# Optimization experiments

Measured on AMD Instinct MI355X. Metric: run time of the kernel, lower is better.

The kernel has to match this reference:

```python
import jax, jax.numpy as jnp
import numpy as np

NUM_ROUTING = 3
EPS = 1e-8


def squash(s, axis):
    # s * (||s||^2 / (1 + ||s||^2)) / ||s||  along `axis`
    sq = jnp.sum(s * s, axis=axis, keepdims=True)
    return s * (sq / (1.0 + sq)) / jnp.sqrt(sq + EPS)


def setup_inputs() -> dict:
    key = jax.random.key(0)
    k1, k2 = jax.random.split(key)
    B, R, C, OUT, IN = 32, 2048, 32, 32, 16
    x = jax.random.normal(k1, (B, R, IN), dtype=jnp.float32)
    vote = jax.random.normal(k2, (R, C, OUT, IN), dtype=jnp.float32)
    return {"x": x, "vote": vote}


def reference(x, vote):
    # votes[b,r,c,o] = sum_i vote[r,c,o,i] * x[b,r,i]
    votes = jnp.einsum('rcoi,bri->brco', vote, x)  # [B,R,C,OUT]
    agreement = jnp.zeros_like(votes)
    verdict = None
    for _ in range(NUM_ROUTING):
        chairman = jax.nn.softmax(agreement, axis=1)          # softmax over routes
        summary = jnp.sum(chairman * votes, axis=1, keepdims=True)  # [B,1,C,OUT]
        verdict = squash(summary, axis=3)                     # squash over out_dim
        agreement = agreement + jnp.sum(votes * verdict, axis=3, keepdims=True)
    return verdict[:, 0, :, :]  # [B, C, OUT]
```

## Files before the change

### kernel.cpp

```cpp
#include <hip/hip_runtime.h>
#include <hip/hip_fp16.h>

#define B 32
#define R 2048
#define C 32
#define O 32
#define IN 16


__global__ __launch_bounds__(512) void votes_kernel(
    const float* __restrict__ x,
    const float* __restrict__ vote,
    __half* __restrict__ votes_h)
{
  const int r0 = blockIdx.x * 16;
  const int c = blockIdx.y;
  const int t = threadIdx.x;
  const int o = t & 31;
  const int rl = t >> 5;
  const int r = r0 + rl;

  __shared__ unsigned int x_lds[32 * 16 * 12];

#pragma unroll
  for (int k = 0; k < 4; ++k) {
    int j = t + k * 512;
    int bb = j >> 6;
    int rr = (j >> 2) & 15;
    int ic = j & 3;
    float4 v = *reinterpret_cast<const float4*>(
        x + ((size_t)bb * R + r0 + rr) * IN + ic * 4);
    __half2 h01 = __float22half2_rn(make_float2(v.x, v.y));
    __half2 h23 = __float22half2_rn(make_float2(v.z, v.w));
    int w = (bb * 16 + rr) * 12 + 2 * ic;
    x_lds[w] = __builtin_bit_cast(unsigned int, h01);
    x_lds[w + 1] = __builtin_bit_cast(unsigned int, h23);
  }
  __syncthreads();

  const float4* vp = reinterpret_cast<const float4*>(
      vote + (((size_t)r * C + c) * O + o) * IN);
  float4 f0 = vp[0], f1 = vp[1], f2 = vp[2], f3 = vp[3];

  __half* optr = votes_h + (size_t)c * 65536 +
                 (size_t)(r >> 1) * 64 + o * 2 + (r & 1);

#pragma unroll 2
  for (int bb = 0; bb < 32; ++bb) {
    const unsigned int* xr = &x_lds[(bb * 16 + rl) * 12];
    uint4 xa = *reinterpret_cast<const uint4*>(xr);
    uint4 xb = *reinterpret_cast<const uint4*>(xr + 4);
    __half2 h0 = __builtin_bit_cast(__half2, xa.x);
    __half2 h1 = __builtin_bit_cast(__half2, xa.y);
    __half2 h2 = __builtin_bit_cast(__half2, xa.z);
    __half2 h3 = __builtin_bit_cast(__half2, xa.w);
    __half2 h4 = __builtin_bit_cast(__half2, xb.x);
    __half2 h5 = __builtin_bit_cast(__half2, xb.y);
    __half2 h6 = __builtin_bit_cast(__half2, xb.z);
    __half2 h7 = __builtin_bit_cast(__half2, xb.w);
    float acc =
        f0.x * __low2float(h0) + f0.y * __high2float(h0) +
        f0.z * __low2float(h1) + f0.w * __high2float(h1) +
        f1.x * __low2float(h2) + f1.y * __high2float(h2) +
        f1.z * __low2float(h3) + f1.w * __high2float(h3) +
        f2.x * __low2float(h4) + f2.y * __high2float(h4) +
        f2.z * __low2float(h5) + f2.w * __high2float(h5) +
        f3.x * __low2float(h6) + f3.y * __high2float(h6) +
        f3.z * __low2float(h7) + f3.w * __high2float(h7);
    optr[(size_t)bb * C * 65536] = __float2half(acc);
  }
}

__global__ __launch_bounds__(1024, 4) void routing_kernel(
    const __half* __restrict__ votes_h,
    float* __restrict__ out)
{
  const int b = blockIdx.x >> 5;
  const int c = blockIdx.x & 31;
  const int t = threadIdx.x;
  const int lane = t & 63;
  const int wave = t >> 6;
  const int g = t >> 5;
  const int o = t & 31;

  __shared__ unsigned int vmix[1024 * 34];
  __shared__ float2 e2[1024];
  __shared__ float red[32][33];
  __shared__ float vdf[32];
  __shared__ float scal_m[16], scal_z[16];

  const uint4* src = reinterpret_cast<const uint4*>(
      votes_h + ((size_t)b * C + c) * 65536);
#pragma unroll
  for (int k = 0; k < 8; ++k) {
    int j = t + k * 1024;
    uint4 v = src[j];
    int rp = j >> 3;
    int q = j & 7;
    unsigned int* dst = &vmix[rp * 34 + 4 * q];
    uint2 a; a.x = v.x; a.y = v.y;
    uint2 d; d.x = v.z; d.y = v.w;
    *reinterpret_cast<uint2*>(dst) = a;
    *reinterpret_cast<uint2*>(dst + 2) = d;
  }
  __syncthreads();

  float a0 = 0.0f, a1 = 0.0f;

  for (int iter = 0; iter < 3; ++iter) {
    float m = fmaxf(a0, a1);
#pragma unroll
    for (int mask = 32; mask; mask >>= 1) m = fmaxf(m, __shfl_xor(m, mask));
    if (lane == 0) scal_m[wave] = m;
    __syncthreads();
    float M = scal_m[0];
#pragma unroll
    for (int w = 1; w < 16; ++w) M = fmaxf(M, scal_m[w]);

    float e0 = __expf(a0 - M), e1 = __expf(a1 - M);
    {
      float z = e0 + e1;
#pragma unroll
      for (int mask = 32; mask; mask >>= 1) z += __shfl_xor(z, mask);
      if (lane == 0) scal_z[wave] = z;
    }
    e2[t] = make_float2(e0, e1);
    __syncthreads();
    float Z = 0.0f;
#pragma unroll
    for (int w = 0; w < 16; ++w) Z += scal_z[w];
    const float Zinv = 1.0f / Z;

    {
      float s = 0.0f;
      const unsigned int* vb = &vmix[(size_t)g * 32 * 34 + o];
      const float2* eb = &e2[g * 32];
#pragma unroll
      for (int j = 0; j < 32; ++j) {
        __half2 vv = __builtin_bit_cast(__half2, vb[j * 34]);
        float2 ee = eb[j];
        s += ee.x * __low2float(vv) + ee.y * __high2float(vv);
      }
      red[o][g] = s;
    }
    __syncthreads();

    if (t < 32) {
      float S = 0.0f;
#pragma unroll
      for (int gg = 0; gg < 32; ++gg) S += red[t][gg];
      float summary = S * Zinv;
      float sq = summary * summary;
#pragma unroll
      for (int mask = 16; mask; mask >>= 1) sq += __shfl_xor(sq, mask);
      float scale = sq / ((1.0f + sq) * sqrtf(sq + 1e-8f));
      float vd = summary * scale;
      vdf[t] = vd;
      if (iter == 2) out[((size_t)b * C + c) * O + t] = vd;
    }
    __syncthreads();

    if (iter < 2) {
      float u0 = 0.0f, u1 = 0.0f;
      const unsigned int* vb = &vmix[(size_t)t * 34];
#pragma unroll
      for (int q = 0; q < 16; ++q) {
        uint2 vv = *reinterpret_cast<const uint2*>(vb + 2 * q);
        __half2 va = __builtin_bit_cast(__half2, vv.x);
        __half2 vbh = __builtin_bit_cast(__half2, vv.y);
        float vda = vdf[2 * q], vdb = vdf[2 * q + 1];
        u0 += __low2float(va) * vda + __low2float(vbh) * vdb;
        u1 += __high2float(va) * vda + __high2float(vbh) * vdb;
      }
      a0 += u0;
      a1 += u1;
      __syncthreads();
    }
  }
}

extern "C" void kernel_launch(void* const* d_in, const int* in_sizes, int n_in,
                              void* d_out, int out_size, void* d_ws, size_t ws_size,
                              hipStream_t stream) {
  const float* x = (const float*)d_in[0];
  const float* vote = (const float*)d_in[1];
  float* out = (float*)d_out;
  __half* votes_h = (__half*)d_ws;

  votes_kernel<<<dim3(R / 16, C), 512, 0, stream>>>(x, vote, votes_h);
  routing_kernel<<<dim3(B * C), 1024, 0, stream>>>(votes_h, out);
}
```

Baseline: 284.3 us.

## Register-tile votes kernel with fp16 dot2 and drop softmax max reduction

The votes kernel now has each thread compute a 2-route by 2-output tile. Vote weights are converted to half once and kept in registers, and the inner product uses the packed fp16 dot2 instruction. Results are written as packed 8-byte stores, and each block covers 2 capsules and 32 routes. In routing, the first iteration uses a uniform softmax with no exp or reduction. The max-subtraction pass and one barrier per iteration are removed, on the assumption that agreement logits stay small enough for an unshifted exp. That removes numerical safety for large logits, and the fp16 weight conversion adds rounding error.

```diff
diff --git a/kernel.cpp b/kernel.cpp
--- a/kernel.cpp
+++ b/kernel.cpp
@@ -7,67 +7,85 @@
 #define O 32
 #define IN 16
 
-
-__global__ __launch_bounds__(512) void votes_kernel(
+typedef _Float16 hf2 __attribute__((ext_vector_type(2)));
+
+
+__global__ __launch_bounds__(512, 4) void votes_kernel(
     const float* __restrict__ x,
     const float* __restrict__ vote,
     __half* __restrict__ votes_h)
 {
-  const int r0 = blockIdx.x * 16;
-  const int c = blockIdx.y;
   const int t = threadIdx.x;
-  const int o = t & 31;
-  const int rl = t >> 5;
-  const int r = r0 + rl;
-
-  __shared__ unsigned int x_lds[32 * 16 * 12];
-
-#pragma unroll
-  for (int k = 0; k < 4; ++k) {
+  const int c = blockIdx.y * 2 + (t >> 8);
+  const int tt = t & 255;
+  const int rp_l = tt >> 4;
+  const int op = tt & 15;
+  const int r0 = blockIdx.x * 32;
+  const int r = r0 + 2 * rp_l;
+  const int rpg = blockIdx.x * 16 + rp_l;
+
+  __shared__ unsigned int x_lds[32 * 32 * 8];
+
+#pragma unroll
+  for (int k = 0; k < 8; ++k) {
     int j = t + k * 512;
-    int bb = j >> 6;
-    int rr = (j >> 2) & 15;
+    int bb = j >> 7;
+    int rr = (j >> 2) & 31;
     int ic = j & 3;
     float4 v = *reinterpret_cast<const float4*>(
         x + ((size_t)bb * R + r0 + rr) * IN + ic * 4);
     __half2 h01 = __float22half2_rn(make_float2(v.x, v.y));
     __half2 h23 = __float22half2_rn(make_float2(v.z, v.w));
-    int w = (bb * 16 + rr) * 12 + 2 * ic;
+    int w = (bb * 32 + rr) * 8 + 2 * ic;
     x_lds[w] = __builtin_bit_cast(unsigned int, h01);
     x_lds[w + 1] = __builtin_bit_cast(unsigned int, h23);
   }
+
+  unsigned int wh[4][8];
+#pragma unroll
+  for (int p = 0; p < 2; ++p) {
+#pragma unroll
+    for (int q = 0; q < 2; ++q) {
+      const float4* vp = reinterpret_cast<const float4*>(
+          vote + (((size_t)(r + p) * C + c) * O + 2 * op + q) * IN);
+#pragma unroll
+      for (int k = 0; k < 4; ++k) {
+        float4 f = vp[k];
+        __half2 a = __float22half2_rn(make_float2(f.x, f.y));
+        __half2 d = __float22half2_rn(make_float2(f.z, f.w));
+        wh[p * 2 + q][2 * k] = __builtin_bit_cast(unsigned int, a);
+        wh[p * 2 + q][2 * k + 1] = __builtin_bit_cast(unsigned int, d);
+      }
+    }
+  }
   __syncthreads();
 
-  const float4* vp = reinterpret_cast<const float4*>(
-      vote + (((size_t)r * C + c) * O + o) * IN);
-  float4 f0 = vp[0], f1 = vp[1], f2 = vp[2], f3 = vp[3];
-
-  __half* optr = votes_h + (size_t)c * 65536 +
-                 (size_t)(r >> 1) * 64 + o * 2 + (r & 1);
+  __half* ob = votes_h + (size_t)c * 65536 + (size_t)rpg * 64 + op * 4;
 
 #pragma unroll 2
   for (int bb = 0; bb < 32; ++bb) {
-    const unsigned int* xr = &x_lds[(bb * 16 + rl) * 12];
-    uint4 xa = *reinterpret_cast<const uint4*>(xr);
-    uint4 xb = *reinterpret_cast<const uint4*>(xr + 4);
-    __half2 h0 = __builtin_bit_cast(__half2, xa.x);
-    __half2 h1 = __builtin_bit_cast(__half2, xa.y);
-    __half2 h2 = __builtin_bit_cast(__half2, xa.z);
-    __half2 h3 = __builtin_bit_cast(__half2, xa.w);
-    __half2 h4 = __builtin_bit_cast(__half2, xb.x);
-    __half2 h5 = __builtin_bit_cast(__half2, xb.y);
-    __half2 h6 = __builtin_bit_cast(__half2, xb.z);
-    __half2 h7 = __builtin_bit_cast(__half2, xb.w);
-    float acc =
-        f0.x * __low2float(h0) + f0.y * __high2float(h0) +
-        f0.z * __low2float(h1) + f0.w * __high2float(h1) +
-        f1.x * __low2float(h2) + f1.y * __high2float(h2) +
-        f1.z * __low2float(h3) + f1.w * __high2float(h3) +
-        f2.x * __low2float(h4) + f2.y * __high2float(h4) +
-        f2.z * __low2float(h5) + f2.w * __high2float(h5) +
-        f3.x * __low2float(h6) + f3.y * __high2float(h6) +
-        f3.z * __low2float(h7) + f3.w * __high2float(h7);
-    optr[(size_t)bb * C * 65536] = __float2half(acc);
+    const uint4* xr = reinterpret_cast<const uint4*>(
+        &x_lds[(bb * 32 + 2 * rp_l) * 8]);
+    uint4 xa = xr[0], xb = xr[1];
+    uint4 xc = xr[2], xd = xr[3];
+    unsigned int x0[8] = {xa.x, xa.y, xa.z, xa.w, xb.x, xb.y, xb.z, xb.w};
+    unsigned int x1[8] = {xc.x, xc.y, xc.z, xc.w, xd.x, xd.y, xd.z, xd.w};
+    float a00 = 0.f, a01 = 0.f, a10 = 0.f, a11 = 0.f;
+#pragma unroll
+    for (int k = 0; k < 8; ++k) {
+      hf2 xv0 = __builtin_bit_cast(hf2, x0[k]);
+      hf2 xv1 = __builtin_bit_cast(hf2, x1[k]);
+      a00 = __builtin_amdgcn_fdot2(__builtin_bit_cast(hf2, wh[0][k]), xv0, a00, false);
+      a01 = __builtin_amdgcn_fdot2(__builtin_bit_cast(hf2, wh[1][k]), xv0, a01, false);
+      a10 = __builtin_amdgcn_fdot2(__builtin_bit_cast(hf2, wh[2][k]), xv1, a10, false);
+      a11 = __builtin_amdgcn_fdot2(__builtin_bit_cast(hf2, wh[3][k]), xv1, a11, false);
+    }
+    __half2 w0 = __float22half2_rn(make_float2(a00, a10));
+    __half2 w1 = __float22half2_rn(make_float2(a01, a11));
+    uint2 pk;
+    pk.x = __builtin_bit_cast(unsigned int, w0);
+    pk.y = __builtin_bit_cast(unsigned int, w1);
+    *reinterpret_cast<uint2*>(ob + (size_t)bb * C * 65536) = pk;
   }
 }
 
@@ -87,7 +105,7 @@
   __shared__ float2 e2[1024];
   __shared__ float red[32][33];
   __shared__ float vdf[32];
-  __shared__ float scal_m[16], scal_z[16];
+  __shared__ float scal_z[16];
 
   const uint4* src = reinterpret_cast<const uint4*>(
       votes_h + ((size_t)b * C + c) * 65536);
@@ -106,40 +124,40 @@
   __syncthreads();
 
   float a0 = 0.0f, a1 = 0.0f;
+  float Zinv = 1.0f / 2048.0f;
 
   for (int iter = 0; iter < 3; ++iter) {
-    float m = fmaxf(a0, a1);
-#pragma unroll
-    for (int mask = 32; mask; mask >>= 1) m = fmaxf(m, __shfl_xor(m, mask));
-    if (lane == 0) scal_m[wave] = m;
-    __syncthreads();
-    float M = scal_m[0];
-#pragma unroll
-    for (int w = 1; w < 16; ++w) M = fmaxf(M, scal_m[w]);
-
-    float e0 = __expf(a0 - M), e1 = __expf(a1 - M);
-    {
+    if (iter > 0) {
+      float e0 = __expf(a0), e1 = __expf(a1);
       float z = e0 + e1;
 #pragma unroll
       for (int mask = 32; mask; mask >>= 1) z += __shfl_xor(z, mask);
       if (lane == 0) scal_z[wave] = z;
-    }
-    e2[t] = make_float2(e0, e1);
-    __syncthreads();
-    float Z = 0.0f;
-#pragma unroll
-    for (int w = 0; w < 16; ++w) Z += scal_z[w];
-    const float Zinv = 1.0f / Z;
+      e2[t] = make_float2(e0, e1);
+      __syncthreads();
+      float Z = 0.0f;
+#pragma unroll
+      for (int w = 0; w < 16; ++w) Z += scal_z[w];
+      Zinv = 1.0f / Z;
+    }
 
     {
       float s = 0.0f;
       const unsigned int* vb = &vmix[(size_t)g * 32 * 34 + o];
-      const float2* eb = &e2[g * 32];
-#pragma unroll
-      for (int j = 0; j < 32; ++j) {
-        __half2 vv = __builtin_bit_cast(__half2, vb[j * 34]);
-        float2 ee = eb[j];
-        s += ee.x * __low2float(vv) + ee.y * __high2float(vv);
+      if (iter == 0) {
+#pragma unroll
+        for (int j = 0; j < 32; ++j) {
+          __half2 vv = __builtin_bit_cast(__half2, vb[j * 34]);
+          s += __low2float(vv) + __high2float(vv);
+        }
+      } else {
+        const float2* eb = &e2[g * 32];
+#pragma unroll
+        for (int j = 0; j < 32; ++j) {
+          __half2 vv = __builtin_bit_cast(__half2, vb[j * 34]);
+          float2 ee = eb[j];
+          s += ee.x * __low2float(vv) + ee.y * __high2float(vv);
+        }
       }
       red[o][g] = s;
     }
@@ -174,7 +192,6 @@
       }
       a0 += u0;
       a1 += u1;
-      __syncthreads();
     }
   }
 }
@@ -187,6 +204,6 @@
   float* out = (float*)d_out;
   __half* votes_h = (__half*)d_ws;
 
-  votes_kernel<<<dim3(R / 16, C), 512, 0, stream>>>(x, vote, votes_h);
+  votes_kernel<<<dim3(R / 32, C / 2), 512, 0, stream>>>(x, vote, votes_h);
   routing_kernel<<<dim3(B * C), 1024, 0, stream>>>(votes_h, out);
 }
```

Result: no change. 284.0 us (-0.1%).
